# Optimization experiments

Measured on AMD Instinct MI355X. Metric: run time of the kernel, lower is better.

Reference implementation:

```python
import jax, jax.numpy as jnp
import numpy as np

N_C, N_F = 25000, 100000   # coarse / fine node counts
E_C, E_F = 100000, 400000  # coarse / fine edge counts
W, F_IN, F_OUT = 128, 128, 4


def _fnn2(x, w1, b1, w2, b2):
    # 2-layer FNN (fnns_depth=2) with SELU, dropout=0 (eval)
    return jax.nn.selu(x @ w1 + b1) @ w2 + b2


def _interaction(v, e, src, dst, n, ew1, eb1, ew2, eb2, nw1, nb1, nw2, nb2):
    # InteractionNetwork: edge update (gather) -> mean scatter -> node update, residuals
    e = _fnn2(jnp.concatenate([e, v[src], v[dst]], axis=-1), ew1, eb1, ew2, eb2) + e
    s = jax.ops.segment_sum(e, dst, num_segments=n)
    cnt = jax.ops.segment_sum(jnp.ones((e.shape[0], 1), e.dtype), dst, num_segments=n)
    agg = s / jnp.maximum(cnt, 1.0)  # 'mean' aggregation
    v = _fnn2(jnp.concatenate([v, agg], axis=-1), nw1, nb1, nw2, nb2) + v
    return v, e


def setup_inputs() -> dict:
    key = jax.random.key(0)
    ks = iter(jax.random.split(key, 64))
    def rn(shape, scale=1.0):
        return jax.random.normal(next(ks), shape, jnp.float32) * scale
    s3, s2, s1 = 1.0 / np.sqrt(3 * W), 1.0 / np.sqrt(2 * W), 1.0 / np.sqrt(W)
    d = {
        'v': rn((N_C, F_IN)),
        'c_coarse': rn((N_C, W)), 'c_fine': rn((N_F, W)),
        'e_coarse': rn((E_C, W)), 'e_fine': rn((E_F, W)),
        'rel_dist': rn((N_F, 1)),
        'ei_coarse': jax.random.randint(next(ks), (2, E_C), 0, N_C),
        'ei_fine': jax.random.randint(next(ks), (2, E_F), 0, N_F),
        'cluster': jax.random.randint(next(ks), (N_F,), 0, N_C),
        'in_node_w': rn((F_IN, W), 1.0 / np.sqrt(F_IN)), 'in_node_b': rn((W,), 0.01),
        'cond_w': rn((2, W, W), s1), 'cond_b': rn((2, W), 0.01),
        'edge_in_w': rn((2, W, W), s1), 'edge_in_b': rn((2, W), 0.01),
        'bn_ew1': rn((2, 3 * W, W), s3), 'bn_eb1': rn((2, W), 0.01),
        'bn_ew2': rn((2, W, W), s1), 'bn_eb2': rn((2, W), 0.01),
        'bn_nw1': rn((2, 2 * W, W), s2), 'bn_nb1': rn((2, W), 0.01),
        'bn_nw2': rn((2, W, W), s1), 'bn_nb2': rn((2, W), 0.01),
        'unp_w1': rn((W + 1, W), 1.0 / np.sqrt(W + 1)), 'unp_b1': rn((W,), 0.01),
        'unp_w2': rn((W, W), s1), 'unp_b2': rn((W,), 0.01),
        'up_ew1': rn((2, 3 * W, W), s3), 'up_eb1': rn((2, W), 0.01),
        'up_ew2': rn((2, W, W), s1), 'up_eb2': rn((2, W), 0.01),
        'up_nw1': rn((2, 2 * W, W), s2), 'up_nb1': rn((2, W), 0.01),
        'up_nw2': rn((2, W, W), s1), 'up_nb2': rn((2, W), 0.01),
        'out_w': rn((W, F_OUT), s1), 'out_b': rn((F_OUT,), 0.01),
    }
    return d


def reference(v, c_coarse, c_fine, e_coarse, e_fine, rel_dist, ei_coarse, ei_fine, cluster,
              in_node_w, in_node_b, cond_w, cond_b, edge_in_w, edge_in_b,
              bn_ew1, bn_eb1, bn_ew2, bn_eb2, bn_nw1, bn_nb1, bn_nw2, bn_nb2,
              unp_w1, unp_b1, unp_w2, unp_b2,
              up_ew1, up_eb1, up_ew2, up_eb2, up_nw1, up_nb1, up_nw2, up_nb2,
              out_w, out_b):
    src_c, dst_c = ei_coarse[0], ei_coarse[1]
    src_f, dst_f = ei_fine[0], ei_fine[1]
    # input projection + coarse-scale conditioning
    v = v @ in_node_w + in_node_b
    v = v + (c_coarse @ cond_w[0] + cond_b[0])
    e = e_coarse @ edge_in_w[0] + edge_in_b[0]
    # bottleneck InteractionNetwork blocks on coarse graph
    for i in range(bn_ew1.shape[0]):
        v, e = _interaction(v, e, src_c, dst_c, N_C,
                            bn_ew1[i], bn_eb1[i], bn_ew2[i], bn_eb2[i],
                            bn_nw1[i], bn_nb1[i], bn_nw2[i], bn_nb2[i])
    # up block: project skip conditioning/edges, unpool coarse->fine via cluster gather + FNN on [v, scalar rel pos]
    c = c_fine @ cond_w[1] + cond_b[1]
    e = e_fine @ edge_in_w[1] + edge_in_b[1]
    v = _fnn2(jnp.concatenate([v[cluster], rel_dist], axis=-1), unp_w1, unp_b1, unp_w2, unp_b2)
    v = v + c
    for i in range(up_ew1.shape[0]):
        v, e = _interaction(v, e, src_f, dst_f, N_F,
                            up_ew1[i], up_eb1[i], up_ew2[i], up_eb2[i],
                            up_nw1[i], up_nb1[i], up_nw2[i], up_nb2[i])
    return v @ out_w + out_b
```

## Files before the change

kernel.cpp:

```cpp
#include <hip/hip_runtime.h>
#include <hip/hip_bf16.h>

typedef __bf16 bf16_t;
typedef __bf16 bf16x8 __attribute__((ext_vector_type(8)));
typedef float f32x4 __attribute__((ext_vector_type(4)));

#define SELU_SCALE 1.0507009873554805f
#define SELU_ALPHA 1.6732632423543772f

__device__ __forceinline__ float selu_f(float x) {
    return x > 0.0f ? SELU_SCALE * x : SELU_SCALE * SELU_ALPHA * (__expf(x) - 1.0f);
}

__device__ __forceinline__ int4 load8(const void* p, size_t elem_off, int isf) {
    if (!isf) return *(const int4*)((const bf16_t*)p + elem_off);
    const float* f = (const float*)p + elem_off;
    float4 a = ((const float4*)f)[0], b = ((const float4*)f)[1];
    union { int4 i; bf16_t h[8]; } u;
    u.h[0] = (bf16_t)a.x; u.h[1] = (bf16_t)a.y; u.h[2] = (bf16_t)a.z; u.h[3] = (bf16_t)a.w;
    u.h[4] = (bf16_t)b.x; u.h[5] = (bf16_t)b.y; u.h[6] = (bf16_t)b.z; u.h[7] = (bf16_t)b.w;
    return u.i;
}

__global__ void detect_dtype(const unsigned short* p, int* flag) {
    if (threadIdx.x == 0) {
        float m = 0.0f;
        for (int i = 0; i < 128; i++) {
            unsigned int u = ((unsigned int)p[i]) << 16;
            float v = __uint_as_float(u);
            v = fabsf(v);
            if (!(v <= 1e3f)) { m = 1e30f; break; }
            m = fmaxf(m, v);
        }
        *flag = (m > 1e3f) ? 1 : 0;
    }
}

struct VDesc { const void* s; bf16_t* d; int eoff; int n; };
struct VArgs { VDesc v[19]; };
__global__ void convert_vecs(VArgs a, const int* __restrict__ flag) {
    int isf = *flag;
    VDesc vd = a.v[blockIdx.y];
    int i = blockIdx.x * 256 + threadIdx.x;
    if (i < vd.n) {
        size_t idx = (size_t)vd.eoff + i;
        vd.d[i] = isf ? (bf16_t)(((const float*)vd.s)[idx]) : ((const bf16_t*)vd.s)[idx];
    }
}

struct TDesc { const void* s; bf16_t* d; int eoff; int Ksrc; int Ktot; int koff; };
struct TArgs { TDesc t[31]; };
__global__ void transpose_all(TArgs a, const int* __restrict__ flag) {
    int isf = *flag;
    TDesc td = a.t[blockIdx.y];
    int i = blockIdx.x * 256 + threadIdx.x;
    if (i < 128 * td.Ksrc) {
        int n = i / td.Ksrc;
        int k = i - n * td.Ksrc;
        size_t si = (size_t)td.eoff + (size_t)k * 128 + n;
        bf16_t v = isf ? (bf16_t)(((const float*)td.s)[si]) : ((const bf16_t*)td.s)[si];
        td.d[(size_t)n * td.Ktot + td.koff + k] = v;
    }
}

__global__ void count_dst2(const int* __restrict__ d0, int* __restrict__ c0, int E0,
                           const int* __restrict__ d1, int* __restrict__ c1, int E1) {
    const int* dst = blockIdx.y ? d1 : d0;
    int* cnt = blockIdx.y ? c1 : c0;
    int E = blockIdx.y ? E1 : E0;
    int e = blockIdx.x * 256 + threadIdx.x;
    if (e < E) atomicAdd(&cnt[dst[e]], 1);
}

__global__ void seg_alloc2(const int* __restrict__ c0, int* __restrict__ rp0, int* __restrict__ cu0, int n0,
                           const int* __restrict__ c1, int* __restrict__ rp1, int* __restrict__ cu1, int n1,
                           int* __restrict__ totals) {
    const int* cnt = blockIdx.y ? c1 : c0;
    int* rp = blockIdx.y ? rp1 : rp0;
    int* cu = blockIdx.y ? cu1 : cu0;
    int n = blockIdx.y ? n1 : n0;
    int* total = totals + blockIdx.y;
    int i = blockIdx.x * 256 + threadIdx.x;
    if (i < n) { int s = atomicAdd(total, cnt[i]); rp[i] = s; cu[i] = s; }
}

__global__ void csr_scatter2(const int* __restrict__ d0, int* __restrict__ cu0, int* __restrict__ e0, int E0,
                             const int* __restrict__ d1, int* __restrict__ cu1, int* __restrict__ e1, int E1) {
    const int* dst = blockIdx.y ? d1 : d0;
    int* cur = blockIdx.y ? cu1 : cu0;
    int* eids = blockIdx.y ? e1 : e0;
    int E = blockIdx.y ? E1 : E0;
    int e = blockIdx.x * 256 + threadIdx.x;
    if (e < E) {
        unsigned s = (unsigned)atomicAdd(&cur[dst[e]], 1);
        if (s < (unsigned)E) eids[s] = e;
    }
}

__global__ void permute_ends2(const int* __restrict__ e0, const int* __restrict__ s0,
                              const int* __restrict__ d0, int* __restrict__ sp0,
                              int* __restrict__ dp0, int E0,
                              const int* __restrict__ e1, const int* __restrict__ s1,
                              const int* __restrict__ d1, int* __restrict__ sp1,
                              int* __restrict__ dp1, int E1) {
    const int* eids = blockIdx.y ? e1 : e0;
    const int* src = blockIdx.y ? s1 : s0;
    const int* dst = blockIdx.y ? d1 : d0;
    int* sp = blockIdx.y ? sp1 : sp0;
    int* dp = blockIdx.y ? dp1 : dp0;
    int E = blockIdx.y ? E1 : E0;
    int s = blockIdx.x * 256 + threadIdx.x;
    if (s < E) { int e = eids[s]; sp[s] = src[e]; dp[s] = dst[e]; }
}

template<int K, int N>
__global__ __launch_bounds__(256) void lin1(
    int M, const void* __restrict__ A0, const void* __restrict__ A1,
    const int* __restrict__ gi,
    const bf16_t* __restrict__ Wt, const bf16_t* __restrict__ b1,
    const bf16_t* __restrict__ b2, const bf16_t* __restrict__ res,
    bf16_t* __restrict__ out, const int* __restrict__ flag)
{
    constexpr int SA = K + 8;
    constexpr int NCT = N / 64;
    __shared__ bf16_t sA[64 * SA];
    const int isf = *flag;
    const int tid = threadIdx.x;
    const int row0 = blockIdx.x * 64;
    const int lane16 = tid & 15;
    const int rgrp = tid >> 4;

    #pragma unroll
    for (int chunk = 0; chunk < K; chunk += 128) {
        const void* sp = chunk ? A1 : A0;
        for (int r = rgrp; r < 64; r += 16) {
            int rr = row0 + r; if (rr >= M) rr = M - 1;
            if (gi) rr = gi[rr];
            int4 u = load8(sp, (size_t)rr * 128 + lane16 * 8, isf);
            *(int4*)&sA[r * SA + chunk + lane16 * 8] = u;
        }
    }
    __syncthreads();

    const int lane = tid & 63, wave = tid >> 6;
    const int l15 = lane & 15, lk = lane >> 4;
    const int colbase = wave * (N / 4);
    f32x4 acc[4][NCT];
    const f32x4 zero = {0.f, 0.f, 0.f, 0.f};
    for (int rt = 0; rt < 4; rt++)
        for (int ct = 0; ct < NCT; ct++) acc[rt][ct] = zero;

    #pragma unroll
    for (int k0 = 0; k0 < K; k0 += 32) {
        bf16x8 wv[NCT];
        #pragma unroll
        for (int ct = 0; ct < NCT; ct++)
            wv[ct] = *(const bf16x8*)(Wt + (size_t)(colbase + ct * 16 + l15) * K + k0 + lk * 8);
        #pragma unroll
        for (int rt = 0; rt < 4; rt++) {
            bf16x8 av = *(const bf16x8*)(&sA[(rt * 16 + l15) * SA + k0 + lk * 8]);
            #pragma unroll
            for (int ct = 0; ct < NCT; ct++)
                acc[rt][ct] = __builtin_amdgcn_mfma_f32_16x16x32_bf16(av, wv[ct], acc[rt][ct], 0, 0, 0);
        }
    }

    #pragma unroll
    for (int rt = 0; rt < 4; rt++)
        #pragma unroll
        for (int ct = 0; ct < NCT; ct++) {
            int col = colbase + ct * 16 + l15;
            float bc = (float)b1[col] + (b2 ? (float)b2[col] : 0.0f);
            #pragma unroll
            for (int r = 0; r < 4; r++) {
                int grow = row0 + rt * 16 + lk * 4 + r;
                if (grow < M) {
                    float x = acc[rt][ct][r] + bc;
                    if (res) x += (float)res[(size_t)grow * N + col];
                    out[(size_t)grow * N + col] = (bf16_t)x;
                }
            }
        }
}

template<int MODE, int INPROJ>
__global__ __launch_bounds__(512, 8) void fnn2k(
    int M,
    const bf16_t* __restrict__ A0, const bf16_t* __restrict__ Psd,
    const int* __restrict__ g0, const int* __restrict__ g1,
    const bf16_t* __restrict__ Emat, const int* __restrict__ rp,
    const int* __restrict__ degc,
    const void* __restrict__ Araw, const int* __restrict__ gie,
    const bf16_t* __restrict__ W0t, const bf16_t* __restrict__ b0,
    const bf16_t* __restrict__ W1t, const bf16_t* __restrict__ b1,
    const bf16_t* __restrict__ W2t, const bf16_t* __restrict__ b2,
    const bf16_t* __restrict__ relb, const bf16_t* __restrict__ w1last,
    const bf16_t* __restrict__ res, bf16_t* __restrict__ out,
    const bf16_t* __restrict__ finw, const bf16_t* __restrict__ finb,
    void* __restrict__ fout, const int* __restrict__ flag)
{
    constexpr int NP = (MODE == 3 && !INPROJ) ? 1 : 2;
    constexpr int K1 = (MODE == 2) ? 256 : 128;
    constexpr int PL = 64 * 136;
    __shared__ bf16_t sA[NP * PL];
    bf16_t* sH = sA + (NP - 1) * PL;

    const int isf = *flag;
    const int tid = threadIdx.x;
    const int lane16 = tid & 15;
    const int rgrp = tid >> 4;
    const int lane = tid & 63, wave = tid >> 6;
    const int l15 = lane & 15, lk = lane >> 4;
    const int colbase = wave * 16;
    const int row0 = blockIdx.x * 64;
    const bool res_lds = (res == A0);
    const f32x4 zero = {0.f, 0.f, 0.f, 0.f};

    #pragma unroll
    for (int c = 0; c < NP; c++) {
        #pragma unroll
        for (int i = 0; i < 2; i++) {
            int r = rgrp + i * 32;
            int rr = row0 + r; if (rr >= M) rr = M - 1;
            int4 u;
            if (MODE == 1 && INPROJ && c == 0) {
                int rr2 = gie[rr];
                u = load8(Araw, (size_t)rr2 * 128 + lane16 * 8, isf);
            } else if (MODE == 1 && c == 1) {
                bf16x8 pa = *(const bf16x8*)(Psd + (size_t)g0[rr] * 256 + lane16 * 8);
                bf16x8 pb = *(const bf16x8*)(Psd + (size_t)g1[rr] * 256 + 128 + lane16 * 8);
                union { int4 i4; bf16_t h[8]; } w;
                #pragma unroll
                for (int j = 0; j < 8; j++) w.h[j] = (bf16_t)((float)pa[j] + (float)pb[j]);
                u = w.i4;
            } else if (MODE == 2 && c == 1) {
                int beg = rp[rr], deg = degc[rr];
                float a8[8] = {0.f, 0.f, 0.f, 0.f, 0.f, 0.f, 0.f, 0.f};
                const bf16_t* ep = Emat + (size_t)beg * 128 + lane16 * 8;
                for (int e = 0; e < deg; e++) {
                    bf16x8 ev = *(const bf16x8*)ep;
                    ep += 128;
                    #pragma unroll
                    for (int j = 0; j < 8; j++) a8[j] += (float)ev[j];
                }
                float inv = 1.0f / (float)(deg > 0 ? deg : 1);
                union { int4 i4; bf16_t h[8]; } w;
                #pragma unroll
                for (int j = 0; j < 8; j++) w.h[j] = (bf16_t)(a8[j] * inv);
                u = w.i4;
            } else if (MODE == 3 && c == 1) {
                u = load8(Araw, (size_t)rr * 128 + lane16 * 8, isf);
            } else {
                const bf16_t* sp = (MODE == 3) ? A0 + (size_t)g0[rr] * 128
                                               : A0 + (size_t)rr * 128;
                u = *(const int4*)(sp + lane16 * 8);
            }
            *(int4*)&sA[c * PL + r * 136 + lane16 * 8] = u;
        }
    }
    __syncthreads();

    f32x4 cC[4] = {zero, zero, zero, zero};
    if constexpr (INPROJ) {
        constexpr int PX = (MODE == 1) ? 0 : 1;
        f32x4 a0r[4];
        #pragma unroll
        for (int rt = 0; rt < 4; rt++) a0r[rt] = zero;
        #pragma unroll
        for (int k0 = 0; k0 < 128; k0 += 32) {
            bf16x8 w0 = *(const bf16x8*)(W0t + (size_t)(colbase + l15) * 128 + k0 + lk * 8);
            #pragma unroll
            for (int rt = 0; rt < 4; rt++) {
                bf16x8 av = *(const bf16x8*)(&sA[PX * PL + (rt * 16 + l15) * 136 + k0 + lk * 8]);
                a0r[rt] = __builtin_amdgcn_mfma_f32_16x16x32_bf16(av, w0, a0r[rt], 0, 0, 0);
            }
        }
        __syncthreads();
        int col = colbase + l15;
        float b0c = (float)b0[col];
        if constexpr (MODE == 1) {
            #pragma unroll
            for (int rt = 0; rt < 4; rt++)
                #pragma unroll
                for (int r = 0; r < 4; r++) {
                    int lrow = rt * 16 + lk * 4 + r;
                    sA[lrow * 136 + col] = (bf16_t)(a0r[rt][r] + b0c);
                }
            __syncthreads();
        } else {
            #pragma unroll
            for (int rt = 0; rt < 4; rt++)
                #pragma unroll
                for (int r = 0; r < 4; r++) cC[rt][r] = a0r[rt][r] + b0c;
        }
    }

    f32x4 acc[4];
    #pragma unroll
    for (int rt = 0; rt < 4; rt++) acc[rt] = zero;
    #pragma unroll
    for (int k0 = 0; k0 < K1; k0 += 32) {
        bf16x8 w0 = *(const bf16x8*)(W1t + (size_t)(colbase + l15) * K1 + k0 + lk * 8);
        #pragma unroll
        for (int rt = 0; rt < 4; rt++) {
            bf16x8 av = *(const bf16x8*)(&sA[(k0 / 128) * PL + (rt * 16 + l15) * 136 + (k0 & 127) + lk * 8]);
            acc[rt] = __builtin_amdgcn_mfma_f32_16x16x32_bf16(av, w0, acc[rt], 0, 0, 0);
        }
    }
    if (MODE != 1) __syncthreads();

    {
        int col = colbase + l15;
        float b1c = (float)b1[col];
        float wlc = (MODE == 3) ? (float)w1last[col] : 0.0f;
        #pragma unroll
        for (int rt = 0; rt < 4; rt++)
            #pragma unroll
            for (int r = 0; r < 4; r++) {
                int lrow = rt * 16 + lk * 4 + r;
                int grow = row0 + lrow;
                float x = acc[rt][r] + b1c;
                if (MODE == 1) x += (float)sH[lrow * 136 + col];
                if (MODE == 3) {
                    float rv = (grow < M) ? (float)relb[grow] : 0.0f;
                    x += rv * wlc;
                }
                x = selu_f(x);
                sH[lrow * 136 + col] = (bf16_t)x;
            }
    }
    __syncthreads();

    f32x4 acc2[4];
    #pragma unroll
    for (int rt = 0; rt < 4; rt++) acc2[rt] = zero;
    #pragma unroll
    for (int k0 = 0; k0 < 128; k0 += 32) {
        bf16x8 w0 = *(const bf16x8*)(W2t + (size_t)(colbase + l15) * 128 + k0 + lk * 8);
        #pragma unroll
        for (int rt = 0; rt < 4; rt++) {
            bf16x8 av = *(const bf16x8*)(&sH[(rt * 16 + l15) * 136 + k0 + lk * 8]);
            acc2[rt] = __builtin_amdgcn_mfma_f32_16x16x32_bf16(av, w0, acc2[rt], 0, 0, 0);
        }
    }
    if (finw) __syncthreads();

    {
        int col = colbase + l15;
        float b2c = (float)b2[col];
        #pragma unroll
        for (int rt = 0; rt < 4; rt++)
            #pragma unroll
            for (int r = 0; r < 4; r++) {
                int lrow = rt * 16 + lk * 4 + r;
                int grow = row0 + lrow;
                if (grow < M) {
                    float x = acc2[rt][r] + b2c;
                    if constexpr (MODE == 3 && INPROJ) {
                        x += cC[rt][r];
                    }
                    if constexpr (MODE == 1 && INPROJ) {
                        x += (float)sA[lrow * 136 + col];
                    } else {
                        if (res) {
                            float rv = (res_lds && NP > 1) ? (float)sA[lrow * 136 + col]
                                                           : (float)res[(size_t)grow * 128 + col];
                            x += rv;
                        }
                    }
                    bf16_t xb = (bf16_t)x;
                    if (out) out[(size_t)grow * 128 + col] = xb;
                    if (finw) sH[lrow * 136 + col] = xb;
                }
            }
    }

    if (finw) {
        __syncthreads();
        if (tid < 256) {
            int orow = tid >> 2, c = tid & 3;
            int grow = row0 + orow;
            if (grow < M) {
                float s = (float)finb[c];
                #pragma unroll
                for (int k = 0; k < 128; k++)
                    s += (float)sH[orow * 136 + k] * (float)finw[k * 4 + c];
                if (isf) ((float*)fout)[(size_t)grow * 4 + c] = s;
                else     ((bf16_t*)fout)[(size_t)grow * 4 + c] = (bf16_t)s;
            }
        }
    }
}

extern "C" void kernel_launch(void* const* d_in, const int* in_sizes, int n_in,
                              void* d_out, int out_size, void* d_ws, size_t ws_size,
                              hipStream_t stream) {
    const int NC = 25000, NF = 100000, EC = 100000, EF = 400000;

    const void* v_in      = d_in[0];
    const void* c_coarse  = d_in[1];
    const void* c_fine    = d_in[2];
    const void* e_coarse  = d_in[3];
    const void* e_fine    = d_in[4];
    const void* rel_dist  = d_in[5];
    const int*  ei_c      = (const int*)d_in[6];
    const int*  ei_f      = (const int*)d_in[7];
    const int*  cluster   = (const int*)d_in[8];
    const void* in_node_w = d_in[9];
    const void* in_node_b = d_in[10];
    const void* cond_w    = d_in[11];
    const void* cond_b    = d_in[12];
    const void* edge_in_w = d_in[13];
    const void* edge_in_b = d_in[14];
    const void* bn_ew1    = d_in[15];
    const void* bn_eb1    = d_in[16];
    const void* bn_ew2    = d_in[17];
    const void* bn_eb2    = d_in[18];
    const void* bn_nw1    = d_in[19];
    const void* bn_nb1    = d_in[20];
    const void* bn_nw2    = d_in[21];
    const void* bn_nb2    = d_in[22];
    const void* unp_w1    = d_in[23];
    const void* unp_b1    = d_in[24];
    const void* unp_w2    = d_in[25];
    const void* unp_b2    = d_in[26];
    const void* up_ew1    = d_in[27];
    const void* up_eb1    = d_in[28];
    const void* up_ew2    = d_in[29];
    const void* up_eb2    = d_in[30];
    const void* up_nw1    = d_in[31];
    const void* up_nb1    = d_in[32];
    const void* up_nw2    = d_in[33];
    const void* up_nb2    = d_in[34];
    const void* out_w     = d_in[35];
    const void* out_b     = d_in[36];

    const int* src_c = ei_c, * dst_c = ei_c + EC;
    const int* src_f = ei_f, * dst_f = ei_f + EF;

    char* base = (char*)d_ws;
    size_t off = 0;
    auto carve = [&](size_t bytes) -> void* {
        void* p = base + off;
        off += (bytes + 255) & ~(size_t)255;
        return p;
    };
    int*    flag   = (int*)carve(256);
    int*    zflag  = (int*)carve(256);
    int*    totals = (int*)carve(256);
    bf16_t* vc     = (bf16_t*)carve((size_t)NC * 128 * 2);
    bf16_t* vf     = (bf16_t*)carve((size_t)NF * 128 * 2);
    bf16_t* ef     = (bf16_t*)carve((size_t)EF * 128 * 2);
    bf16_t* ec     = ef;
    bf16_t* Psd    = (bf16_t*)carve((size_t)NF * 256 * 2);
    int*    cnti_c = (int*)carve((size_t)NC * 4);
    int*    cnti_f = (int*)carve((size_t)NF * 4);
    int*    rp_c   = (int*)carve((size_t)NC * 4);
    int*    rp_f   = (int*)carve((size_t)NF * 4);
    int*    cur_c  = (int*)carve((size_t)NC * 4);
    int*    cur_f  = (int*)carve((size_t)NF * 4);
    int*    srcp_c = (int*)carve((size_t)EC * 4);
    int*    dstp_c = (int*)carve((size_t)EC * 4);
    int*    srcp_f = (int*)carve((size_t)EF * 4);
    int*    dstp_f = (int*)carve((size_t)EF * 4);

    auto cw = [&](size_t elems) -> bf16_t* { return (bf16_t*)carve(elems * 2); };
    bf16_t* Wic    = cw(128 * 256);
    bf16_t* Wein0  = cw(128 * 128);
    bf16_t* Wein1  = cw(128 * 128);
    bf16_t* Wcond1 = cw(128 * 128);
    bf16_t* Wbe1[2] = { cw(128 * 128), cw(128 * 128) };
    bf16_t* Wsd_c[2] = { cw(256 * 128), cw(256 * 128) };
    bf16_t* Wbe2[2] = { cw(128 * 128), cw(128 * 128) };
    bf16_t* Wbn1[2] = { cw(128 * 256), cw(128 * 256) };
    bf16_t* Wbn2[2] = { cw(128 * 128), cw(128 * 128) };
    bf16_t* Wunp1 = cw(128 * 128);
    bf16_t* Wunp2 = cw(128 * 128);
    bf16_t* Wue1[2] = { cw(128 * 128), cw(128 * 128) };
    bf16_t* Wsd_f[2] = { cw(256 * 128), cw(256 * 128) };
    bf16_t* Wue2[2] = { cw(128 * 128), cw(128 * 128) };
    bf16_t* Wun1[2] = { cw(128 * 256), cw(128 * 256) };
    bf16_t* Wun2[2] = { cw(128 * 128), cw(128 * 128) };
    bf16_t* b_in   = cw(128);
    bf16_t* b_cond = cw(256);
    bf16_t* b_ein  = cw(256);
    bf16_t* b_be1  = cw(256);
    bf16_t* b_be2  = cw(256);
    bf16_t* b_bn1  = cw(256);
    bf16_t* b_bn2  = cw(256);
    bf16_t* b_unp1 = cw(128);
    bf16_t* b_unp2 = cw(128);
    bf16_t* b_ue1  = cw(256);
    bf16_t* b_ue2  = cw(256);
    bf16_t* b_un1  = cw(256);
    bf16_t* b_un2  = cw(256);
    bf16_t* b_out  = cw(8);
    bf16_t* w1last = cw(128);
    bf16_t* relb   = cw(NF);
    bf16_t* foutw  = cw(512);
    bf16_t* zerob  = cw(256);
    int*    eids_c = (int*)carve((size_t)EC * 4);
    int*    eids_f = (int*)carve((size_t)EF * 4);

    detect_dtype<<<1, 64, 0, stream>>>((const unsigned short*)in_node_b, flag);
    hipMemsetAsync(zflag, 0, 256, stream);
    hipMemsetAsync(zerob, 0, 512, stream);

    VArgs va; int vi = 0;
    auto addV = [&](const void* s, bf16_t* d, int eoff, int n) {
        va.v[vi].s = s; va.v[vi].d = d; va.v[vi].eoff = eoff; va.v[vi].n = n; vi++;
    };
    addV(in_node_b, b_in, 0, 128);
    addV(cond_b, b_cond, 0, 256);
    addV(edge_in_b, b_ein, 0, 256);
    addV(bn_eb1, b_be1, 0, 256);  addV(bn_eb2, b_be2, 0, 256);
    addV(bn_nb1, b_bn1, 0, 256);  addV(bn_nb2, b_bn2, 0, 256);
    addV(unp_b1, b_unp1, 0, 128); addV(unp_b2, b_unp2, 0, 128);
    addV(up_eb1, b_ue1, 0, 256);  addV(up_eb2, b_ue2, 0, 256);
    addV(up_nb1, b_un1, 0, 256);  addV(up_nb2, b_un2, 0, 256);
    addV(out_b, b_out, 0, 4);
    addV(unp_w1, w1last, 128 * 128, 128);
    addV(rel_dist, relb, 0, NF);
    addV(out_w, foutw, 0, 512);
    dim3 vg((NF + 255) / 256, vi);
    convert_vecs<<<vg, 256, 0, stream>>>(va, flag);

    TArgs ta; int ti = 0;
    auto addT = [&](const void* s, bf16_t* d, int eoff, int Ksrc, int Ktot, int koff) {
        ta.t[ti].s = s; ta.t[ti].d = d; ta.t[ti].eoff = eoff;
        ta.t[ti].Ksrc = Ksrc; ta.t[ti].Ktot = Ktot; ta.t[ti].koff = koff; ti++;
    };
    addT(in_node_w, Wic, 0, 128, 256, 0);
    addT(cond_w,    Wic, 0, 128, 256, 128);
    addT(edge_in_w, Wein0, 0, 128, 128, 0);
    addT(edge_in_w, Wein1, 16384, 128, 128, 0);
    addT(cond_w,    Wcond1, 16384, 128, 128, 0);
    for (int i = 0; i < 2; i++) {
        addT(bn_ew1, Wbe1[i],           i * 49152,         128, 128, 0);
        addT(bn_ew1, Wsd_c[i],          i * 49152 + 16384, 128, 128, 0);
        addT(bn_ew1, Wsd_c[i] + 16384,  i * 49152 + 32768, 128, 128, 0);
        addT(bn_ew2, Wbe2[i], i * 16384, 128, 128, 0);
        addT(bn_nw1, Wbn1[i], i * 32768, 256, 256, 0);
        addT(bn_nw2, Wbn2[i], i * 16384, 128, 128, 0);
        addT(up_ew1, Wue1[i],           i * 49152,         128, 128, 0);
        addT(up_ew1, Wsd_f[i],          i * 49152 + 16384, 128, 128, 0);
        addT(up_ew1, Wsd_f[i] + 16384,  i * 49152 + 32768, 128, 128, 0);
        addT(up_ew2, Wue2[i], i * 16384, 128, 128, 0);
        addT(up_nw1, Wun1[i], i * 32768, 256, 256, 0);
        addT(up_nw2, Wun2[i], i * 16384, 128, 128, 0);
    }
    addT(unp_w1, Wunp1, 0, 128, 128, 0);
    addT(unp_w2, Wunp2, 0, 128, 128, 0);
    dim3 tg((128 * 256 + 255) / 256, ti);
    transpose_all<<<tg, 256, 0, stream>>>(ta, flag);

    hipMemsetAsync(cnti_c, 0, (size_t)NC * 4, stream);
    hipMemsetAsync(cnti_f, 0, (size_t)NF * 4, stream);
    hipMemsetAsync(totals, 0, 256, stream);
    dim3 ge((EF + 255) / 256, 2), gn((NF + 255) / 256, 2);
    count_dst2<<<ge, 256, 0, stream>>>(dst_c, cnti_c, EC, dst_f, cnti_f, EF);
    seg_alloc2<<<gn, 256, 0, stream>>>(cnti_c, rp_c, cur_c, NC, cnti_f, rp_f, cur_f, NF, totals);
    csr_scatter2<<<ge, 256, 0, stream>>>(dst_c, cur_c, eids_c, EC, dst_f, cur_f, eids_f, EF);
    permute_ends2<<<ge, 256, 0, stream>>>(eids_c, src_c, dst_c, srcp_c, dstp_c, EC,
                                          eids_f, src_f, dst_f, srcp_f, dstp_f, EF);

    lin1<256, 128><<<(NC + 63) / 64, 256, 0, stream>>>(NC, v_in, c_coarse, nullptr, Wic,
                                                       b_in, b_cond, nullptr, vc, flag);

    lin1<128, 256><<<(NC + 63) / 64, 256, 0, stream>>>(NC, vc, nullptr, nullptr, Wsd_c[0],
                                                       zerob, nullptr, nullptr, Psd, zflag);
    fnn2k<1, 1><<<(EC + 63) / 64, 512, 0, stream>>>(
        EC, nullptr, Psd, srcp_c, dstp_c, nullptr, nullptr, nullptr,
        e_coarse, eids_c, Wein0, b_ein,
        Wbe1[0], b_be1, Wbe2[0], b_be2,
        nullptr, nullptr, nullptr, ec, nullptr, nullptr, nullptr, flag);
    fnn2k<2, 0><<<(NC + 63) / 64, 512, 0, stream>>>(
        NC, vc, nullptr, nullptr, nullptr, ec, rp_c, cnti_c,
        nullptr, nullptr, nullptr, nullptr,
        Wbn1[0], b_bn1, Wbn2[0], b_bn2,
        nullptr, nullptr, vc, vc, nullptr, nullptr, nullptr, flag);
    lin1<128, 256><<<(NC + 63) / 64, 256, 0, stream>>>(NC, vc, nullptr, nullptr, Wsd_c[1],
                                                       zerob, nullptr, nullptr, Psd, zflag);
    fnn2k<1, 0><<<(EC + 63) / 64, 512, 0, stream>>>(
        EC, ec, Psd, srcp_c, dstp_c, nullptr, nullptr, nullptr,
        nullptr, nullptr, nullptr, nullptr,
        Wbe1[1], b_be1 + 128, Wbe2[1], b_be2 + 128,
        nullptr, nullptr, ec, ec, nullptr, nullptr, nullptr, flag);
    fnn2k<2, 0><<<(NC + 63) / 64, 512, 0, stream>>>(
        NC, vc, nullptr, nullptr, nullptr, ec, rp_c, cnti_c,
        nullptr, nullptr, nullptr, nullptr,
        Wbn1[1], b_bn1 + 128, Wbn2[1], b_bn2 + 128,
        nullptr, nullptr, vc, vc, nullptr, nullptr, nullptr, flag);

    fnn2k<3, 1><<<(NF + 63) / 64, 512, 0, stream>>>(
        NF, vc, nullptr, cluster, nullptr, nullptr, nullptr, nullptr,
        c_fine, nullptr, Wcond1, b_cond + 128,
        Wunp1, b_unp1, Wunp2, b_unp2,
        relb, w1last, nullptr, vf, nullptr, nullptr, nullptr, flag);

    lin1<128, 256><<<(NF + 63) / 64, 256, 0, stream>>>(NF, vf, nullptr, nullptr, Wsd_f[0],
                                                       zerob, nullptr, nullptr, Psd, zflag);
    fnn2k<1, 1><<<(EF + 63) / 64, 512, 0, stream>>>(
        EF, nullptr, Psd, srcp_f, dstp_f, nullptr, nullptr, nullptr,
        e_fine, eids_f, Wein1, b_ein + 128,
        Wue1[0], b_ue1, Wue2[0], b_ue2,
        nullptr, nullptr, nullptr, ef, nullptr, nullptr, nullptr, flag);
    fnn2k<2, 0><<<(NF + 63) / 64, 512, 0, stream>>>(
        NF, vf, nullptr, nullptr, nullptr, ef, rp_f, cnti_f,
        nullptr, nullptr, nullptr, nullptr,
        Wun1[0], b_un1, Wun2[0], b_un2,
        nullptr, nullptr, vf, vf, nullptr, nullptr, nullptr, flag);
    lin1<128, 256><<<(NF + 63) / 64, 256, 0, stream>>>(NF, vf, nullptr, nullptr, Wsd_f[1],
                                                       zerob, nullptr, nullptr, Psd, zflag);
    fnn2k<1, 0><<<(EF + 63) / 64, 512, 0, stream>>>(
        EF, ef, Psd, srcp_f, dstp_f, nullptr, nullptr, nullptr,
        nullptr, nullptr, nullptr, nullptr,
        Wue1[1], b_ue1 + 128, Wue2[1], b_ue2 + 128,
        nullptr, nullptr, ef, ef, nullptr, nullptr, nullptr, flag);
    fnn2k<2, 0><<<(NF + 63) / 64, 512, 0, stream>>>(
        NF, vf, nullptr, nullptr, nullptr, ef, rp_f, cnti_f,
        nullptr, nullptr, nullptr, nullptr,
        Wun1[1], b_un1 + 128, Wun2[1], b_un2 + 128,
        nullptr, nullptr, vf, nullptr,
        foutw, b_out, d_out, flag);
}
```

Before: 729.2 us.

## Process edges in original order and gather via CSR edge ids in aggregation

Removes the permute kernel that reordered edge endpoints by destination, so edge FNN kernels consume edges in their original order and read input edge features directly without an index indirection. The node aggregation kernel now looks up edge ids from the CSR list and gathers scattered edge rows instead of reading a contiguous sorted segment. This saves one preprocessing kernel and temp buffers but gives up locality in both the destination-node gathers and the segment reduction.

```diff
diff --git a/kernel.cpp b/kernel.cpp
--- a/kernel.cpp
+++ b/kernel.cpp
@@ -97,26 +97,9 @@
     }
 }
 
-__global__ void permute_ends2(const int* __restrict__ e0, const int* __restrict__ s0,
-                              const int* __restrict__ d0, int* __restrict__ sp0,
-                              int* __restrict__ dp0, int E0,
-                              const int* __restrict__ e1, const int* __restrict__ s1,
-                              const int* __restrict__ d1, int* __restrict__ sp1,
-                              int* __restrict__ dp1, int E1) {
-    const int* eids = blockIdx.y ? e1 : e0;
-    const int* src = blockIdx.y ? s1 : s0;
-    const int* dst = blockIdx.y ? d1 : d0;
-    int* sp = blockIdx.y ? sp1 : sp0;
-    int* dp = blockIdx.y ? dp1 : dp0;
-    int E = blockIdx.y ? E1 : E0;
-    int s = blockIdx.x * 256 + threadIdx.x;
-    if (s < E) { int e = eids[s]; sp[s] = src[e]; dp[s] = dst[e]; }
-}
-
 template<int K, int N>
 __global__ __launch_bounds__(256) void lin1(
     int M, const void* __restrict__ A0, const void* __restrict__ A1,
-    const int* __restrict__ gi,
     const bf16_t* __restrict__ Wt, const bf16_t* __restrict__ b1,
     const bf16_t* __restrict__ b2, const bf16_t* __restrict__ res,
     bf16_t* __restrict__ out, const int* __restrict__ flag)
@@ -135,7 +118,6 @@
         const void* sp = chunk ? A1 : A0;
         for (int r = rgrp; r < 64; r += 16) {
             int rr = row0 + r; if (rr >= M) rr = M - 1;
-            if (gi) rr = gi[rr];
             int4 u = load8(sp, (size_t)rr * 128 + lane16 * 8, isf);
             *(int4*)&sA[r * SA + chunk + lane16 * 8] = u;
         }
@@ -189,8 +171,8 @@
     const bf16_t* __restrict__ A0, const bf16_t* __restrict__ Psd,
     const int* __restrict__ g0, const int* __restrict__ g1,
     const bf16_t* __restrict__ Emat, const int* __restrict__ rp,
-    const int* __restrict__ degc,
-    const void* __restrict__ Araw, const int* __restrict__ gie,
+    const int* __restrict__ degc, const int* __restrict__ eids,
+    const void* __restrict__ Araw,
     const bf16_t* __restrict__ W0t, const bf16_t* __restrict__ b0,
     const bf16_t* __restrict__ W1t, const bf16_t* __restrict__ b1,
     const bf16_t* __restrict__ W2t, const bf16_t* __restrict__ b2,
@@ -224,8 +206,7 @@
             int rr = row0 + r; if (rr >= M) rr = M - 1;
             int4 u;
             if (MODE == 1 && INPROJ && c == 0) {
-                int rr2 = gie[rr];
-                u = load8(Araw, (size_t)rr2 * 128 + lane16 * 8, isf);
+                u = load8(Araw, (size_t)rr * 128 + lane16 * 8, isf);
             } else if (MODE == 1 && c == 1) {
                 bf16x8 pa = *(const bf16x8*)(Psd + (size_t)g0[rr] * 256 + lane16 * 8);
                 bf16x8 pb = *(const bf16x8*)(Psd + (size_t)g1[rr] * 256 + 128 + lane16 * 8);
@@ -236,10 +217,9 @@
             } else if (MODE == 2 && c == 1) {
                 int beg = rp[rr], deg = degc[rr];
                 float a8[8] = {0.f, 0.f, 0.f, 0.f, 0.f, 0.f, 0.f, 0.f};
-                const bf16_t* ep = Emat + (size_t)beg * 128 + lane16 * 8;
                 for (int e = 0; e < deg; e++) {
-                    bf16x8 ev = *(const bf16x8*)ep;
-                    ep += 128;
+                    int eid = eids[beg + e];
+                    bf16x8 ev = *(const bf16x8*)(Emat + (size_t)eid * 128 + lane16 * 8);
                     #pragma unroll
                     for (int j = 0; j < 8; j++) a8[j] += (float)ev[j];
                 }
@@ -459,10 +439,6 @@
     int*    rp_f   = (int*)carve((size_t)NF * 4);
     int*    cur_c  = (int*)carve((size_t)NC * 4);
     int*    cur_f  = (int*)carve((size_t)NF * 4);
-    int*    srcp_c = (int*)carve((size_t)EC * 4);
-    int*    dstp_c = (int*)carve((size_t)EC * 4);
-    int*    srcp_f = (int*)carve((size_t)EF * 4);
-    int*    dstp_f = (int*)carve((size_t)EF * 4);
 
     auto cw = [&](size_t elems) -> bf16_t* { return (bf16_t*)carve(elems * 2); };
     bf16_t* Wic    = cw(128 * 256);
@@ -561,65 +537,63 @@
     count_dst2<<<ge, 256, 0, stream>>>(dst_c, cnti_c, EC, dst_f, cnti_f, EF);
     seg_alloc2<<<gn, 256, 0, stream>>>(cnti_c, rp_c, cur_c, NC, cnti_f, rp_f, cur_f, NF, totals);
     csr_scatter2<<<ge, 256, 0, stream>>>(dst_c, cur_c, eids_c, EC, dst_f, cur_f, eids_f, EF);
-    permute_ends2<<<ge, 256, 0, stream>>>(eids_c, src_c, dst_c, srcp_c, dstp_c, EC,
-                                          eids_f, src_f, dst_f, srcp_f, dstp_f, EF);
-
-    lin1<256, 128><<<(NC + 63) / 64, 256, 0, stream>>>(NC, v_in, c_coarse, nullptr, Wic,
+
+    lin1<256, 128><<<(NC + 63) / 64, 256, 0, stream>>>(NC, v_in, c_coarse, Wic,
                                                        b_in, b_cond, nullptr, vc, flag);
 
-    lin1<128, 256><<<(NC + 63) / 64, 256, 0, stream>>>(NC, vc, nullptr, nullptr, Wsd_c[0],
+    lin1<128, 256><<<(NC + 63) / 64, 256, 0, stream>>>(NC, vc, nullptr, Wsd_c[0],
                                                        zerob, nullptr, nullptr, Psd, zflag);
     fnn2k<1, 1><<<(EC + 63) / 64, 512, 0, stream>>>(
-        EC, nullptr, Psd, srcp_c, dstp_c, nullptr, nullptr, nullptr,
-        e_coarse, eids_c, Wein0, b_ein,
+        EC, nullptr, Psd, src_c, dst_c, nullptr, nullptr, nullptr, nullptr,
+        e_coarse, Wein0, b_ein,
         Wbe1[0], b_be1, Wbe2[0], b_be2,
         nullptr, nullptr, nullptr, ec, nullptr, nullptr, nullptr, flag);
     fnn2k<2, 0><<<(NC + 63) / 64, 512, 0, stream>>>(
-        NC, vc, nullptr, nullptr, nullptr, ec, rp_c, cnti_c,
-        nullptr, nullptr, nullptr, nullptr,
+        NC, vc, nullptr, nullptr, nullptr, ec, rp_c, cnti_c, eids_c,
+        nullptr, nullptr, nullptr,
         Wbn1[0], b_bn1, Wbn2[0], b_bn2,
         nullptr, nullptr, vc, vc, nullptr, nullptr, nullptr, flag);
-    lin1<128, 256><<<(NC + 63) / 64, 256, 0, stream>>>(NC, vc, nullptr, nullptr, Wsd_c[1],
+    lin1<128, 256><<<(NC + 63) / 64, 256, 0, stream>>>(NC, vc, nullptr, Wsd_c[1],
                                                        zerob, nullptr, nullptr, Psd, zflag);
     fnn2k<1, 0><<<(EC + 63) / 64, 512, 0, stream>>>(
-        EC, ec, Psd, srcp_c, dstp_c, nullptr, nullptr, nullptr,
-        nullptr, nullptr, nullptr, nullptr,
+        EC, ec, Psd, src_c, dst_c, nullptr, nullptr, nullptr, nullptr,
+        nullptr, nullptr, nullptr,
         Wbe1[1], b_be1 + 128, Wbe2[1], b_be2 + 128,
         nullptr, nullptr, ec, ec, nullptr, nullptr, nullptr, flag);
     fnn2k<2, 0><<<(NC + 63) / 64, 512, 0, stream>>>(
-        NC, vc, nullptr, nullptr, nullptr, ec, rp_c, cnti_c,
-        nullptr, nullptr, nullptr, nullptr,
+        NC, vc, nullptr, nullptr, nullptr, ec, rp_c, cnti_c, eids_c,
+        nullptr, nullptr, nullptr,
         Wbn1[1], b_bn1 + 128, Wbn2[1], b_bn2 + 128,
         nullptr, nullptr, vc, vc, nullptr, nullptr, nullptr, flag);
 
     fnn2k<3, 1><<<(NF + 63) / 64, 512, 0, stream>>>(
-        NF, vc, nullptr, cluster, nullptr, nullptr, nullptr, nullptr,
-        c_fine, nullptr, Wcond1, b_cond + 128,
+        NF, vc, nullptr, cluster, nullptr, nullptr, nullptr, nullptr, nullptr,
+        c_fine, Wcond1, b_cond + 128,
         Wunp1, b_unp1, Wunp2, b_unp2,
         relb, w1last, nullptr, vf, nullptr, nullptr, nullptr, flag);
 
-    lin1<128, 256><<<(NF + 63) / 64, 256, 0, stream>>>(NF, vf, nullptr, nullptr, Wsd_f[0],
+    lin1<128, 256><<<(NF + 63) / 64, 256, 0, stream>>>(NF, vf, nullptr, Wsd_f[0],
                                                        zerob, nullptr, nullptr, Psd, zflag);
     fnn2k<1, 1><<<(EF + 63) / 64, 512, 0, stream>>>(
-        EF, nullptr, Psd, srcp_f, dstp_f, nullptr, nullptr, nullptr,
-        e_fine, eids_f, Wein1, b_ein + 128,
+        EF, nullptr, Psd, src_f, dst_f, nullptr, nullptr, nullptr, nullptr,
+        e_fine, Wein1, b_ein + 128,
         Wue1[0], b_ue1, Wue2[0], b_ue2,
         nullptr, nullptr, nullptr, ef, nullptr, nullptr, nullptr, flag);
     fnn2k<2, 0><<<(NF + 63) / 64, 512, 0, stream>>>(
-        NF, vf, nullptr, nullptr, nullptr, ef, rp_f, cnti_f,
-        nullptr, nullptr, nullptr, nullptr,
+        NF, vf, nullptr, nullptr, nullptr, ef, rp_f, cnti_f, eids_f,
+        nullptr, nullptr, nullptr,
         Wun1[0], b_un1, Wun2[0], b_un2,
         nullptr, nullptr, vf, vf, nullptr, nullptr, nullptr, flag);
-    lin1<128, 256><<<(NF + 63) / 64, 256, 0, stream>>>(NF, vf, nullptr, nullptr, Wsd_f[1],
+    lin1<128, 256><<<(NF + 63) / 64, 256, 0, stream>>>(NF, vf, nullptr, Wsd_f[1],
                                                        zerob, nullptr, nullptr, Psd, zflag);
     fnn2k<1, 0><<<(EF + 63) / 64, 512, 0, stream>>>(
-        EF, ef, Psd, srcp_f, dstp_f, nullptr, nullptr, nullptr,
-        nullptr, nullptr, nullptr, nullptr,
+        EF, ef, Psd, src_f, dst_f, nullptr, nullptr, nullptr, nullptr,
+        nullptr, nullptr, nullptr,
         Wue1[1], b_ue1 + 128, Wue2[1], b_ue2 + 128,
         nullptr, nullptr, ef, ef, nullptr, nullptr, nullptr, flag);
     fnn2k<2, 0><<<(NF + 63) / 64, 512, 0, stream>>>(
-        NF, vf, nullptr, nullptr, nullptr, ef, rp_f, cnti_f,
-        nullptr, nullptr, nullptr, nullptr,
+        NF, vf, nullptr, nullptr, nullptr, ef, rp_f, cnti_f, eids_f,
+        nullptr, nullptr, nullptr,
         Wun1[1], b_un1 + 128, Wun2[1], b_un2 + 128,
         nullptr, nullptr, vf, nullptr,
         foutw, b_out, d_out, flag);
```

New measurement: 744.0 us. 2.0% more time.
